# Optimization experiments

Measured on AMD Instinct MI355X. Metric: run time of the kernel, lower is better.

## Reference

```python
import jax, jax.numpy as jnp
import numpy as np

COMMITMENT_COST = 0.25


def setup_inputs() -> dict:
    key = jax.random.key(0)
    k1, k2 = jax.random.split(key)
    ze = jax.random.normal(k1, (16, 256, 32, 32), dtype=jnp.float32)
    codebook = jax.random.normal(k2, (8192, 256), dtype=jnp.float32) * 0.02
    return {"ze": ze, "codebook": codebook}


def reference(ze, codebook):
    # ze: [B, C, H, W] -> [B, H, W, C]
    B, C, H, W = ze.shape
    ze_nhwc = jnp.transpose(ze, (0, 2, 3, 1))
    ze_flat = ze_nhwc.reshape(B * H * W, C)

    # squared L2 distances to every codebook row: [B*H*W, vocab]
    distances = (
        jnp.sum(ze_flat ** 2, axis=1, keepdims=True)
        + jnp.sum(codebook ** 2, axis=1)
        - 2.0 * ze_flat @ codebook.T
    )
    encoding_indices = jnp.argmin(distances, axis=1)  # [B*H*W]
    zq = codebook[encoding_indices].reshape(B, H, W, C)

    sg = jax.lax.stop_gradient
    quantization_loss = jnp.mean((sg(ze_nhwc) - zq) ** 2)
    commitment_loss = jnp.mean((ze_nhwc - sg(zq)) ** 2)
    vq_loss = quantization_loss + COMMITMENT_COST * commitment_loss

    # straight-through estimator (training mode)
    zq = ze_nhwc + sg(zq - ze_nhwc)
    zq = jnp.transpose(zq, (0, 3, 1, 2))  # back to [B, C, H, W]
    return vq_loss, zq, encoding_indices.reshape(B, H * W)
```

## Files before the change

kernel.cpp:

```cpp
#include <hip/hip_runtime.h>
#include <hip/hip_bf16.h>

#define NPIX 16384
#define NVOC 8192
#define CHUNK 32

typedef short short8v __attribute__((ext_vector_type(8)));
typedef float floatx4 __attribute__((ext_vector_type(4)));

#define WS_ZEBF   0u
#define WS_BLIST  0u
#define WS_PART   0u
#define WS_CBBF   8388608u
#define WS_PK     8388608u
#define WS_TAU    8519680u
#define WS_ZEF    12582912u
#define WS_MIN    29360128u
#define WS_BN     37748736u
#define WS_AN     37781504u
#define WS_BCNT   37847040u
#define WS_BMAXU  37847552u
#define WS_QCNT   37847556u
#define WS_QUEUE  37847808u

__device__ __forceinline__ short f2bf(float v) {
  __bf16 h = (__bf16)v;
  return __builtin_bit_cast(short, h);
}

__device__ __forceinline__ unsigned long long packdj(float d, int j) {
  return ((unsigned long long)__float_as_uint(d) << 32) | (unsigned int)j;
}

__device__ __forceinline__ void gll16(const void* g, void* l) {
  __builtin_amdgcn_global_load_lds(
      (const __attribute__((address_space(1))) void*)g,
      (__attribute__((address_space(3))) void*)l, 16, 0, 0);
}

__device__ __forceinline__ float np_pairwise128_sq(const float* x, int stride) {
  float r[8];
#pragma unroll
  for (int j = 0; j < 8; ++j) {
    float v = x[j * stride];
    r[j] = __fmul_rn(v, v);
  }
#pragma unroll
  for (int i = 1; i < 16; ++i) {
#pragma unroll
    for (int j = 0; j < 8; ++j) {
      float v = x[(i * 8 + j) * stride];
      r[j] = __fadd_rn(r[j], __fmul_rn(v, v));
    }
  }
  return __fadd_rn(__fadd_rn(__fadd_rn(r[0], r[1]), __fadd_rn(r[2], r[3])),
                   __fadd_rn(__fadd_rn(r[4], r[5]), __fadd_rn(r[6], r[7])));
}

__global__ __launch_bounds__(256) void k_cvt_ze(const float* __restrict__ ze,
                                                short* __restrict__ zebff,
                                                float* __restrict__ zef,
                                                float* __restrict__ an,
                                                unsigned* __restrict__ bmaxu,
                                                int* __restrict__ qcnt) {
  __shared__ float t[64][132];
  int tid = threadIdx.x;
  if (blockIdx.x == 0 && tid == 0) {
    bmaxu[0] = 0u;
    qcnt[0] = 0;
  }
  int p0 = blockIdx.x * 64;
  int b = p0 >> 10, hw0 = p0 & 1023;
  const float* src = ze + (size_t)b * 262144 + hw0;
  float apart = 0.f;
  for (int half = 0; half < 2; ++half) {
    if (half) __syncthreads();
    {
      int hw = tid & 63, cq = tid >> 6;
#pragma unroll
      for (int i = 0; i < 32; ++i) {
        int cl = i * 4 + cq;
        t[hw][cl] = src[(size_t)(half * 128 + cl) * 1024 + hw];
      }
    }
    __syncthreads();
    {
      int r = tid >> 2, cg = tid & 3;
      float* fd = zef + (size_t)(p0 + r) * 256 + half * 128 + cg * 32;
#pragma unroll
      for (int s = 0; s < 8; ++s) {
        float4 v = *reinterpret_cast<const float4*>(&t[r][cg * 32 + s * 4]);
        *reinterpret_cast<float4*>(fd + s * 4) = v;
      }
    }
    {
      int pg_l = tid >> 6, l = tid & 63;
      size_t pg = (size_t)(p0 >> 4) + pg_l;
      int lr = l & 15, lg = l >> 4;
#pragma unroll
      for (int kl = 0; kl < 4; ++kl) {
        int ks = half * 4 + kl;
        short8v v8;
#pragma unroll
        for (int e = 0; e < 8; ++e)
          v8[e] = f2bf(t[pg_l * 16 + lr][kl * 32 + lg * 8 + e]);
        *reinterpret_cast<short8v*>(zebff + (pg * 8 + ks) * 512 + l * 8) = v8;
      }
    }
    if (tid < 64) {
      float a = np_pairwise128_sq(&t[tid][0], 1);
      apart = half ? __fadd_rn(apart, a) : a;
    }
  }
  if (tid < 64) an[p0 + tid] = apart;
}

__global__ __launch_bounds__(256) void k_cvt_cb(const float* __restrict__ cb,
                                                short* __restrict__ cbbft,
                                                float* __restrict__ bn,
                                                unsigned* __restrict__ bmaxu) {
  __shared__ float rows[64][257];
  int tid = threadIdx.x;
  int j0 = blockIdx.x * 64;
  for (int r = 0; r < 64; ++r)
    rows[r][tid] = cb[(size_t)(j0 + r) * 256 + tid];
  __syncthreads();
  if (tid < 64) {
    float a = np_pairwise128_sq(&rows[tid][0], 1);
    float b2 = np_pairwise128_sq(&rows[tid][128], 1);
    float v = __fadd_rn(a, b2);
    bn[j0 + tid] = v;
    atomicMax(bmaxu, __float_as_uint(v));
  }
  short* dst = cbbft + (size_t)blockIdx.x * 16384;
#pragma unroll
  for (int s = 0; s < 8; ++s) {
    int cid = tid + s * 256;
    int kc = cid >> 6, c2 = cid & 63;
    short8v v;
#pragma unroll
    for (int e = 0; e < 8; ++e) v[e] = f2bf(rows[c2][kc * 8 + e]);
    *reinterpret_cast<short8v*>(dst + cid * 8) = v;
  }
}

__global__ __launch_bounds__(256, 2) void k_gemm(const short* __restrict__ zebff,
                                                 const short* __restrict__ cbbft,
                                                 const float* __restrict__ bn,
                                                 float* __restrict__ wsmin) {
  __shared__ short lds[32768];
  __shared__ float bnlds[1024];
  int tid = threadIdx.x;
  int lane = tid & 63, w = tid >> 6;
  int g = lane >> 4, r16 = lane & 15;
  int oct = blockIdx.x & 7, chunk = blockIdx.x >> 3;
  int p0 = chunk * 256;
  int ncol0 = oct * 1024;

  short8v pix[4][8];
  {
    const short* base = zebff + ((size_t)(p0 >> 4) + w * 4) * 4096 + lane * 8;
#pragma unroll
    for (int pf = 0; pf < 4; ++pf)
#pragma unroll
      for (int ks = 0; ks < 8; ++ks)
        pix[pf][ks] =
            *reinterpret_cast<const short8v*>(base + pf * 4096 + ks * 512);
  }
  gll16(bn + ncol0 + tid * 4, &bnlds[tid * 4]);

#define STAGE(t, boff)                                                         \
  {                                                                            \
    const short* src_ = cbbft + (size_t)(oct * 16 + (t)) * 16384;              \
    _Pragma("unroll") for (int s = 0; s < 8; ++s) {                            \
      int cid_ = tid + s * 256;                                                \
      gll16(src_ + cid_ * 8, &lds[(boff) + cid_ * 8]);                         \
    }                                                                          \
  }
  STAGE(0, 0)
  asm volatile("s_waitcnt vmcnt(0)" ::: "memory");
  __builtin_amdgcn_s_barrier();

  float* wbase = wsmin + (size_t)(oct * 16) * NPIX + p0 + w * 64 + r16;

  for (int t = 0; t < 16; ++t) {
    int bA = (t & 1) * 16384;
    int bC = bA ^ 16384;
    if (t < 15) STAGE(t + 1, bC)
    float4 bnv[4];
#pragma unroll
    for (int cf = 0; cf < 4; ++cf)
      bnv[cf] =
          *reinterpret_cast<const float4*>(&bnlds[t * 64 + cf * 16 + g * 4]);
    floatx4 acc[4][4];
#pragma unroll
    for (int cf = 0; cf < 4; ++cf)
#pragma unroll
      for (int pf = 0; pf < 4; ++pf) acc[cf][pf] = floatx4{0.f, 0.f, 0.f, 0.f};
    __builtin_amdgcn_s_setprio(1);
#pragma unroll
    for (int ks = 0; ks < 8; ++ks) {
      short8v cfr[4];
#pragma unroll
      for (int cf = 0; cf < 4; ++cf)
        cfr[cf] = *reinterpret_cast<const short8v*>(
            &lds[bA + (((ks * 4 + g) * 64) + cf * 16 + r16) * 8]);
#pragma unroll
      for (int cf = 0; cf < 4; ++cf)
#pragma unroll
        for (int pf = 0; pf < 4; ++pf)
          acc[cf][pf] = __builtin_amdgcn_mfma_f32_16x16x32_bf16(
              cfr[cf], pix[pf][ks], acc[cf][pf], 0, 0, 0);
    }
    __builtin_amdgcn_s_setprio(0);
    float pmin[4];
#pragma unroll
    for (int pf = 0; pf < 4; ++pf) {
      float m_ = 3.4e38f;
#pragma unroll
      for (int cf = 0; cf < 4; ++cf) {
        m_ = fminf(m_, __builtin_fmaf(-2.0f, acc[cf][pf][0], bnv[cf].x));
        m_ = fminf(m_, __builtin_fmaf(-2.0f, acc[cf][pf][1], bnv[cf].y));
        m_ = fminf(m_, __builtin_fmaf(-2.0f, acc[cf][pf][2], bnv[cf].z));
        m_ = fminf(m_, __builtin_fmaf(-2.0f, acc[cf][pf][3], bnv[cf].w));
      }
      m_ = fminf(m_, __shfl_xor(m_, 16));
      m_ = fminf(m_, __shfl_xor(m_, 32));
      pmin[pf] = m_;
    }
    if (lane < 16) {
#pragma unroll
      for (int pf = 0; pf < 4; ++pf)
        wbase[(size_t)t * NPIX + pf * 16] = pmin[pf];
    }
    if (t < 15) asm volatile("s_waitcnt vmcnt(4)" ::: "memory");
    __builtin_amdgcn_s_barrier();
  }
#undef STAGE
}

__global__ __launch_bounds__(256) void k_tau(const float* __restrict__ wsmin,
                                             const float* __restrict__ an,
                                             const unsigned* __restrict__ bmaxu,
                                             float* __restrict__ tau,
                                             unsigned long long* __restrict__ pk) {
  __shared__ float sm[4][64];
  int tid = threadIdx.x;
  int px = tid & 63, q = tid >> 6;
  int p = blockIdx.x * 64 + px;
  float m0 = 3.4e38f, m1 = 3.4e38f, m2 = 3.4e38f, m3 = 3.4e38f;
#pragma unroll
  for (int i = 0; i < 8; ++i) {
    int c = q * 32 + i * 4;
    m0 = fminf(m0, wsmin[(size_t)c * NPIX + p]);
    m1 = fminf(m1, wsmin[(size_t)(c + 1) * NPIX + p]);
    m2 = fminf(m2, wsmin[(size_t)(c + 2) * NPIX + p]);
    m3 = fminf(m3, wsmin[(size_t)(c + 3) * NPIX + p]);
  }
  sm[q][px] = fminf(fminf(m0, m1), fminf(m2, m3));
  __syncthreads();
  if (tid < 64) {
    float m = fminf(fminf(sm[0][tid], sm[1][tid]), fminf(sm[2][tid], sm[3][tid]));
    float bmaxf = sqrtf(__uint_as_float(bmaxu[0]));
    tau[p] = m + 0.017f * sqrtf(an[p]) * bmaxf + 2e-4f;
    pk[p] = ~0ull;
  }
}

__global__ __launch_bounds__(256) void k_compact(const float* __restrict__ wsmin,
                                                 const float* __restrict__ tau,
                                                 const float* __restrict__ cb,
                                                 float* __restrict__ cbsw,
                                                 int* __restrict__ bcnt,
                                                 int* __restrict__ blist,
                                                 int* __restrict__ qcnt,
                                                 int* __restrict__ queue) {
  __shared__ int wbase[4];
  __shared__ int running;
  int c = blockIdx.x;
  const float* row = wsmin + (size_t)c * NPIX;
  int* dst = blist + (size_t)c * NPIX;
  int tid = threadIdx.x;
  int lane = tid & 63, wv = tid >> 6;
  if (tid == 0) running = 0;
  __syncthreads();
  for (int base = 0; base < NPIX; base += 256) {
    int p = base + tid;
    bool flag = row[p] <= tau[p];
    unsigned long long mask = __ballot(flag);
    int cnt = __popcll(mask);
    int pre = __popcll(mask & ((1ull << lane) - 1ull));
    if (lane == 0) wbase[wv] = cnt;
    __syncthreads();
    if (tid == 0) {
      int r = running;
#pragma unroll
      for (int w2 = 0; w2 < 4; ++w2) {
        int t = wbase[w2];
        wbase[w2] = r;
        r += t;
      }
      running = r;
    }
    __syncthreads();
    if (flag) dst[wbase[wv] + pre] = p;
    __syncthreads();
  }
  if (tid == 0) {
    int n = running;
    bcnt[c] = n;
    int nch = (n + CHUNK - 1) / CHUNK;
    if (nch > 0) {
      int q0 = atomicAdd(qcnt, nch * 2);
      for (int i = 0; i < nch; ++i) {
        queue[q0 + 2 * i] = (2 * c) | (i << 16);
        queue[q0 + 2 * i + 1] = (2 * c + 1) | (i << 16);
      }
    }
  }
  {
    const float4* cb4 = reinterpret_cast<const float4*>(cb);
    float4* dst4 = reinterpret_cast<float4*>(cbsw);
#pragma unroll
    for (int i = 0; i < 16; ++i) {
      int gid = tid + i * 256;
      int jj = 64 * c + (gid >> 6), u = gid & 63;
      dst4[(size_t)jj * 64 + u] = cb4[(size_t)jj * 64 + (u ^ (jj & 7))];
    }
  }
}

__global__ __launch_bounds__(256, 2) void k_rescore_b(
    const float* __restrict__ zef, const float* __restrict__ cbsw,
    const float* __restrict__ an, const float* __restrict__ bn,
    const int* __restrict__ bcnt, const int* __restrict__ blist,
    const int* __restrict__ qcnt, const int* __restrict__ queue,
    unsigned long long* __restrict__ pk) {
  __shared__ float zl[32 * 256];
  __shared__ float cstf[32 * 256];
  __shared__ int pidx[32];
  __shared__ float apx[32];
  int tid = threadIdx.x;
  int lane = tid & 63, wv = tid >> 6;
  int code32 = lane & 31, half = lane >> 5;
  int nq = qcnt[0];
  for (int qi = blockIdx.x; qi < nq; qi += 512) {
    int e = queue[qi];
    int g = e & 0xffff, chunk = e >> 16;
    int c = g >> 1;
    int n = bcnt[c];
    int base = chunk * CHUNK;
    int cnt_here = min(CHUNK, n - base);
    __syncthreads();
#pragma unroll
    for (int i = 0; i < 8; ++i) {
      int px = wv * 8 + i;
      int idx = base + min(px, cnt_here - 1);
      int p = blist[(size_t)c * NPIX + idx];
      gll16(zef + (size_t)p * 256 + lane * 4, &zl[px * 256 + lane * 4]);
    }
#pragma unroll
    for (int i = 0; i < 8; ++i) {
      int r = wv * 8 + i;
      gll16(cbsw + (size_t)(g * 32 + r) * 256 + lane * 4,
            &cstf[r * 256 + lane * 4]);
    }
    if (tid < 32) {
      int idx = base + min(tid, cnt_here - 1);
      int p = blist[(size_t)c * NPIX + idx];
      pidx[tid] = p;
      apx[tid] = an[p];
    }
    asm volatile("s_waitcnt vmcnt(0)" ::: "memory");
    __syncthreads();
    int jg = g * 32 + code32;
    float bnj = bn[jg];
    int px0 = wv * 8 + half * 4;
    int sw = code32 & 7;
    const float* crow = &cstf[code32 * 256];
    float acc[4] = {0.f, 0.f, 0.f, 0.f};
#pragma unroll 8
    for (int k4 = 0; k4 < 64; ++k4) {
      float4 cv = *reinterpret_cast<const float4*>(&crow[(k4 ^ sw) << 2]);
#pragma unroll
      for (int i = 0; i < 4; ++i) {
        float4 zv =
            *reinterpret_cast<const float4*>(&zl[(px0 + i) * 256 + k4 * 4]);
        acc[i] = __builtin_fmaf(zv.x, cv.x, acc[i]);
        acc[i] = __builtin_fmaf(zv.y, cv.y, acc[i]);
        acc[i] = __builtin_fmaf(zv.z, cv.z, acc[i]);
        acc[i] = __builtin_fmaf(zv.w, cv.w, acc[i]);
      }
    }
#pragma unroll
    for (int i = 0; i < 4; ++i) {
      int px = px0 + i;
      float d = __fsub_rn(__fadd_rn(apx[px], bnj), 2.0f * acc[i]);
      unsigned long long q = packdj(d, jg);
#pragma unroll
      for (int off = 1; off < 32; off <<= 1) {
        unsigned long long q2 = __shfl_xor(q, off);
        q = q2 < q ? q2 : q;
      }
      if (code32 == 0) atomicMin(&pk[pidx[px]], q);
    }
  }
}

__global__ __launch_bounds__(256) void k_gather(const float* __restrict__ ze,
                                                const float* __restrict__ cb,
                                                const unsigned long long* __restrict__ pk,
                                                float* __restrict__ out_zq,
                                                float* __restrict__ out_idx,
                                                float* __restrict__ part) {
  __shared__ float qrow[64][257];
  __shared__ int sidx[64];
  int tid = threadIdx.x;
  int p0 = blockIdx.x * 64;
  int b = p0 >> 10, hw0 = p0 & 1023;
  if (tid < 64) {
    int bi = (int)(unsigned int)(pk[p0 + tid] & 0xffffffffull);
    sidx[tid] = bi;
    out_idx[p0 + tid] = (float)bi;
  }
  __syncthreads();
  for (int r = 0; r < 64; ++r)
    qrow[r][tid] = cb[(size_t)sidx[r] * 256 + tid];
  __syncthreads();
  float lsum = 0.f;
  size_t zbase = (size_t)b * 262144 + hw0;
#pragma unroll 4
  for (int i = 0; i < 64; ++i) {
    int px = tid & 63;
    int c = i * 4 + (tid >> 6);
    float qv = qrow[px][c];
    size_t gi = zbase + (size_t)c * 1024 + px;
    float zev = ze[gi];
    out_zq[gi] = __fadd_rn(zev, __fsub_rn(qv, zev));
    float d = zev - qv;
    lsum = __builtin_fmaf(d, d, lsum);
  }
#pragma unroll
  for (int off = 32; off; off >>= 1) lsum += __shfl_xor(lsum, off, 64);
  __shared__ float wsum[4];
  if ((tid & 63) == 0) wsum[tid >> 6] = lsum;
  __syncthreads();
  if (tid == 0) part[blockIdx.x] = (wsum[0] + wsum[1]) + (wsum[2] + wsum[3]);
}

__global__ __launch_bounds__(256) void k_final(const float* __restrict__ part,
                                               float* __restrict__ out0) {
  int tid = threadIdx.x;
  float s = part[tid];
#pragma unroll
  for (int off = 32; off; off >>= 1) s += __shfl_xor(s, off, 64);
  __shared__ float wsum[4];
  if ((tid & 63) == 0) wsum[tid >> 6] = s;
  __syncthreads();
  if (tid == 0)
    out0[0] = 1.25f * ((wsum[0] + wsum[1]) + (wsum[2] + wsum[3])) / 4194304.0f;
}

extern "C" void kernel_launch(void* const* d_in, const int* in_sizes, int n_in,
                              void* d_out, int out_size, void* d_ws, size_t ws_size,
                              hipStream_t stream) {
  const float* ze = (const float*)d_in[0];
  const float* cb = (const float*)d_in[1];
  float* out = (float*)d_out;
  char* ws = (char*)d_ws;
  short* zebff = (short*)(ws + WS_ZEBF);
  short* cbbft = (short*)(ws + WS_CBBF);
  float* zef = (float*)(ws + WS_ZEF);
  float* bn = (float*)(ws + WS_BN);
  float* an = (float*)(ws + WS_AN);
  float* wsmin = (float*)(ws + WS_MIN);
  float* cbsw = (float*)(ws + WS_MIN);
  float* tau = (float*)(ws + WS_TAU);
  int* blist = (int*)(ws + WS_BLIST);
  int* bcnt = (int*)(ws + WS_BCNT);
  unsigned* bmaxu = (unsigned*)(ws + WS_BMAXU);
  int* qcnt = (int*)(ws + WS_QCNT);
  int* queue = (int*)(ws + WS_QUEUE);
  unsigned long long* pk = (unsigned long long*)(ws + WS_PK);
  float* part = (float*)(ws + WS_PART);
  float* out_loss = out;
  float* out_zq = out + 1;
  float* out_idx = out + 1 + 4194304;

  k_cvt_ze<<<256, 256, 0, stream>>>(ze, zebff, zef, an, bmaxu, qcnt);
  k_cvt_cb<<<128, 256, 0, stream>>>(cb, cbbft, bn, bmaxu);
  k_gemm<<<512, 256, 0, stream>>>(zebff, cbbft, bn, wsmin);
  k_tau<<<256, 256, 0, stream>>>(wsmin, an, bmaxu, tau, pk);
  k_compact<<<128, 256, 0, stream>>>(wsmin, tau, cb, cbsw, bcnt, blist, qcnt,
                                     queue);
  k_rescore_b<<<512, 256, 0, stream>>>(zef, cbsw, an, bn, bcnt, blist, qcnt,
                                       queue, pk);
  k_gather<<<256, 256, 0, stream>>>(ze, cb, pk, out_zq, out_idx, part);
  k_final<<<1, 256, 0, stream>>>(part, out_loss);
}
```

Baseline: 170.7 us.

## Halve GEMM column tile to 32 codes and double grid for occupancy

The distance GEMM block now covers 512 codebook columns in tiles of 32 instead of 1024 columns in tiles of 64. This halves LDS and accumulator registers per block, lets four blocks share a CU, and doubles the grid to 1024 blocks. The codebook conversion kernel re-lays out bf16 tiles to match the 32-column layout. Per-64-column minima are still produced by merging pairs of sub-tiles and packing the writes across lane groups, which keeps the wsmin layout unchanged for downstream kernels. The cost is less codebook reuse per loaded pixel fragment, more barriers per unit of work, and a stricter vmcnt wait on even iterations.

```diff
diff --git a/kernel.cpp b/kernel.cpp
--- a/kernel.cpp
+++ b/kernel.cpp
@@ -135,27 +135,29 @@
   short* dst = cbbft + (size_t)blockIdx.x * 16384;
 #pragma unroll
   for (int s = 0; s < 8; ++s) {
-    int cid = tid + s * 256;
-    int kc = cid >> 6, c2 = cid & 63;
+    int id = tid + s * 256;
+    int th = id >> 10;
+    int rid = id & 1023;
+    int kc = rid >> 5, c2 = rid & 31;
     short8v v;
 #pragma unroll
-    for (int e = 0; e < 8; ++e) v[e] = f2bf(rows[c2][kc * 8 + e]);
-    *reinterpret_cast<short8v*>(dst + cid * 8) = v;
-  }
-}
-
-__global__ __launch_bounds__(256, 2) void k_gemm(const short* __restrict__ zebff,
+    for (int e = 0; e < 8; ++e) v[e] = f2bf(rows[th * 32 + c2][kc * 8 + e]);
+    *reinterpret_cast<short8v*>(dst + id * 8) = v;
+  }
+}
+
+__global__ __launch_bounds__(256, 4) void k_gemm(const short* __restrict__ zebff,
                                                  const short* __restrict__ cbbft,
                                                  const float* __restrict__ bn,
                                                  float* __restrict__ wsmin) {
-  __shared__ short lds[32768];
-  __shared__ float bnlds[1024];
+  __shared__ short lds[16384];
+  __shared__ float bnlds[512];
   int tid = threadIdx.x;
   int lane = tid & 63, w = tid >> 6;
   int g = lane >> 4, r16 = lane & 15;
-  int oct = blockIdx.x & 7, chunk = blockIdx.x >> 3;
+  int seg = blockIdx.x & 15, chunk = blockIdx.x >> 4;
   int p0 = chunk * 256;
-  int ncol0 = oct * 1024;
+  int ncol0 = seg * 512;
 
   short8v pix[4][8];
   {
@@ -167,12 +169,12 @@
         pix[pf][ks] =
             *reinterpret_cast<const short8v*>(base + pf * 4096 + ks * 512);
   }
-  gll16(bn + ncol0 + tid * 4, &bnlds[tid * 4]);
+  if (tid < 128) gll16(bn + ncol0 + tid * 4, &bnlds[tid * 4]);
 
 #define STAGE(t, boff)                                                         \
   {                                                                            \
-    const short* src_ = cbbft + (size_t)(oct * 16 + (t)) * 16384;              \
-    _Pragma("unroll") for (int s = 0; s < 8; ++s) {                            \
+    const short* src_ = cbbft + (size_t)(seg * 16 + (t)) * 8192;               \
+    _Pragma("unroll") for (int s = 0; s < 4; ++s) {                            \
       int cid_ = tid + s * 256;                                                \
       gll16(src_ + cid_ * 8, &lds[(boff) + cid_ * 8]);                         \
     }                                                                          \
@@ -181,32 +183,33 @@
   asm volatile("s_waitcnt vmcnt(0)" ::: "memory");
   __builtin_amdgcn_s_barrier();
 
-  float* wbase = wsmin + (size_t)(oct * 16) * NPIX + p0 + w * 64 + r16;
+  float* wbase = wsmin + (size_t)(seg * 8) * NPIX + p0 + w * 64 + g * 16 + r16;
+  float pminPrev[4];
 
   for (int t = 0; t < 16; ++t) {
-    int bA = (t & 1) * 16384;
-    int bC = bA ^ 16384;
+    int bA = (t & 1) * 8192;
+    int bC = bA ^ 8192;
     if (t < 15) STAGE(t + 1, bC)
-    float4 bnv[4];
-#pragma unroll
-    for (int cf = 0; cf < 4; ++cf)
+    float4 bnv[2];
+#pragma unroll
+    for (int cf = 0; cf < 2; ++cf)
       bnv[cf] =
-          *reinterpret_cast<const float4*>(&bnlds[t * 64 + cf * 16 + g * 4]);
-    floatx4 acc[4][4];
-#pragma unroll
-    for (int cf = 0; cf < 4; ++cf)
+          *reinterpret_cast<const float4*>(&bnlds[t * 32 + cf * 16 + g * 4]);
+    floatx4 acc[2][4];
+#pragma unroll
+    for (int cf = 0; cf < 2; ++cf)
 #pragma unroll
       for (int pf = 0; pf < 4; ++pf) acc[cf][pf] = floatx4{0.f, 0.f, 0.f, 0.f};
     __builtin_amdgcn_s_setprio(1);
 #pragma unroll
     for (int ks = 0; ks < 8; ++ks) {
-      short8v cfr[4];
-#pragma unroll
-      for (int cf = 0; cf < 4; ++cf)
+      short8v cfr[2];
+#pragma unroll
+      for (int cf = 0; cf < 2; ++cf)
         cfr[cf] = *reinterpret_cast<const short8v*>(
-            &lds[bA + (((ks * 4 + g) * 64) + cf * 16 + r16) * 8]);
-#pragma unroll
-      for (int cf = 0; cf < 4; ++cf)
+            &lds[bA + (((ks * 4 + g) * 32) + cf * 16 + r16) * 8]);
+#pragma unroll
+      for (int cf = 0; cf < 2; ++cf)
 #pragma unroll
         for (int pf = 0; pf < 4; ++pf)
           acc[cf][pf] = __builtin_amdgcn_mfma_f32_16x16x32_bf16(
@@ -218,7 +221,7 @@
     for (int pf = 0; pf < 4; ++pf) {
       float m_ = 3.4e38f;
 #pragma unroll
-      for (int cf = 0; cf < 4; ++cf) {
+      for (int cf = 0; cf < 2; ++cf) {
         m_ = fminf(m_, __builtin_fmaf(-2.0f, acc[cf][pf][0], bnv[cf].x));
         m_ = fminf(m_, __builtin_fmaf(-2.0f, acc[cf][pf][1], bnv[cf].y));
         m_ = fminf(m_, __builtin_fmaf(-2.0f, acc[cf][pf][2], bnv[cf].z));
@@ -228,12 +231,18 @@
       m_ = fminf(m_, __shfl_xor(m_, 32));
       pmin[pf] = m_;
     }
-    if (lane < 16) {
-#pragma unroll
-      for (int pf = 0; pf < 4; ++pf)
-        wbase[(size_t)t * NPIX + pf * 16] = pmin[pf];
-    }
-    if (t < 15) asm volatile("s_waitcnt vmcnt(4)" ::: "memory");
+    if (t & 1) {
+      float v = fminf(pminPrev[0], pmin[0]);
+      if (g == 1) v = fminf(pminPrev[1], pmin[1]);
+      if (g == 2) v = fminf(pminPrev[2], pmin[2]);
+      if (g == 3) v = fminf(pminPrev[3], pmin[3]);
+      wbase[(size_t)(t >> 1) * NPIX] = v;
+      asm volatile("s_waitcnt vmcnt(1)" ::: "memory");
+    } else {
+#pragma unroll
+      for (int pf = 0; pf < 4; ++pf) pminPrev[pf] = pmin[pf];
+      asm volatile("s_waitcnt vmcnt(0)" ::: "memory");
+    }
     __builtin_amdgcn_s_barrier();
   }
 #undef STAGE
@@ -489,7 +498,7 @@
 
   k_cvt_ze<<<256, 256, 0, stream>>>(ze, zebff, zef, an, bmaxu, qcnt);
   k_cvt_cb<<<128, 256, 0, stream>>>(cb, cbbft, bn, bmaxu);
-  k_gemm<<<512, 256, 0, stream>>>(zebff, cbbft, bn, wsmin);
+  k_gemm<<<1024, 256, 0, stream>>>(zebff, cbbft, bn, wsmin);
   k_tau<<<256, 256, 0, stream>>>(wsmin, an, bmaxu, tau, pk);
   k_compact<<<128, 256, 0, stream>>>(wsmin, tau, cb, cbsw, bcnt, blist, qcnt,
                                      queue);
```

After: 300.8 us. 76.2% more time.
